# Performance work log

Measured on AMD Instinct MI355X. Metric: run time of the kernel, lower is better.

The kernel has to match this reference:

```python
import jax, jax.numpy as jnp
import numpy as np

BS, C, N, L = 2, 64, 400, 12   # [bs, c, N, L]
D, H = 128, 8                  # model_dim, num_heads
HD = D // H                    # head_dim = 16
FF = 1024                      # feed_forward_dim
EPS_LN = 1e-5
EPS_NORM = 1e-12


def setup_inputs() -> dict:
    key = jax.random.key(0)
    ks = jax.random.split(key, 24)
    w = lambda k, shape: jax.random.normal(k, shape, jnp.float32) * 0.02
    inp = {
        "x":     jax.random.normal(ks[0], (BS, C, N, L), jnp.float32),
        "x_au1": jax.random.normal(ks[1], (BS, C, N, L), jnp.float32),
        "x_au2": jax.random.normal(ks[2], (BS, C, N, L), jnp.float32),
        # projections stored as [in, out] so y = x @ W + b
        "WQ1": w(ks[3], (C, D)),  "bQ1": jnp.zeros((D,)),
        "WQ2": w(ks[4], (C, D)),  "bQ2": jnp.zeros((D,)),
        "WK1": w(ks[5], (C, D)),  "bK1": jnp.zeros((D,)),
        "WK2": w(ks[6], (C, D)),  "bK2": jnp.zeros((D,)),
        "WV":  w(ks[7], (C, D)),  "bV":  jnp.zeros((D,)),
        "Wo":  w(ks[8], (D, C)),  "bo":  jnp.zeros((C,)),
        "Wf1": w(ks[9], (C, FF)), "bf1": jnp.zeros((FF,)),
        "Wf2": w(ks[10], (FF, C)),"bf2": jnp.zeros((C,)),
        "g1": jnp.ones((C,)), "be1": jnp.zeros((C,)),
        "g2": jnp.ones((C,)), "be2": jnp.zeros((C,)),
        "temperature": jnp.ones((H,)),
        "alphas": jnp.ones((2,)) / 2.0,
    }
    return inp


def _layernorm(x, g, b):
    m = jnp.mean(x, axis=-1, keepdims=True)
    v = jnp.var(x, axis=-1, keepdims=True)
    return (x - m) * jax.lax.rsqrt(v + EPS_LN) * g + b


def _l2norm(x):
    n = jnp.linalg.norm(x, axis=-1, keepdims=True)
    return x / jnp.maximum(n, EPS_NORM)


def _topk_masked(attn, k):
    # keep entries >= k-th largest along last axis (ties measure-zero for floats)
    kth = jax.lax.top_k(attn, k)[0][..., -1:]
    return jnp.where(attn >= kth, attn, -jnp.inf)


def reference(x, x_au1, x_au2, WQ1, bQ1, WQ2, bQ2, WK1, bK1, WK2, bK2,
              WV, bV, Wo, bo, Wf1, bf1, Wf2, bf2, g1, be1, g2, be2,
              temperature, alphas):
    # [bs,c,N,L] -> [bs,L,N,c]
    xt  = jnp.transpose(x,     (0, 3, 2, 1))
    a1t = jnp.transpose(x_au1, (0, 3, 2, 1))
    a2t = jnp.transpose(x_au2, (0, 3, 2, 1))
    bs, Lq, Nq, c = xt.shape

    def heads(t):  # [bs,L,N,D] -> [bs,L,N,H,hd]
        return t.reshape(bs, Lq, Nq, H, HD)

    q1 = _l2norm(heads(a1t @ WQ1 + bQ1))
    q2 = _l2norm(heads(a2t @ WQ2 + bQ2))
    k1 = _l2norm(heads(xt  @ WK1 + bK1))
    k2 = _l2norm(heads(xt  @ WK2 + bK2))
    v  = heads(xt @ WV + bV)

    # dual cosine attention scores: [bs,H,L,N,N]
    attn = (jnp.einsum('blnhd,blmhd->bhlnm', q1, k1)
            + jnp.einsum('blnhd,blmhd->bhlnm', q2, k2))
    attn = attn * temperature.reshape(1, H, 1, 1, 1)

    k_top1 = max(1, Nq // 2)
    k_top2 = max(1, Nq // 4)
    p1 = jax.nn.softmax(_topk_masked(attn, k_top1), axis=-1)
    p2 = jax.nn.softmax(_topk_masked(attn, k_top2), axis=-1)

    out1 = jnp.einsum('bhlnm,blmhd->blnhd', p1, v)
    out2 = jnp.einsum('bhlnm,blmhd->blnhd', p2, v)
    al = jax.nn.softmax(alphas)
    out = (out1 * al[0] + out2 * al[1]).reshape(bs, Lq, Nq, D)

    out = out @ Wo + bo
    out = _layernorm(xt + out, g1, be1)
    ff = jax.nn.relu(out @ Wf1 + bf1) @ Wf2 + bf2
    out = _layernorm(out + ff, g2, be2)
    out = jnp.transpose(out, (0, 3, 2, 1))  # back to [bs,c,N,L]

    attn_flat = attn.reshape(bs * H, Lq, Nq, Nq)
    p2_flat = p2.reshape(bs * H, Lq, Nq, Nq)
    return out, attn_flat, p2_flat
```

## Files before the change

### kernel.cpp

```cpp
#include <hip/hip_runtime.h>
#include <math.h>

#define BSZ 2
#define CHN 64
#define NPT 400
#define LW  12
#define DM  128
#define NH  8
#define HDM 16
#define FFD 1024
#define NTOK (BSZ*LW*NPT)

#define TA 16
__global__ __launch_bounds__(128) void stage_a(
    const float* __restrict__ x, const float* __restrict__ xa1, const float* __restrict__ xa2,
    const float* __restrict__ WQ1, const float* __restrict__ bQ1,
    const float* __restrict__ WQ2, const float* __restrict__ bQ2,
    const float* __restrict__ WK1, const float* __restrict__ bK1,
    const float* __restrict__ WK2, const float* __restrict__ bK2,
    const float* __restrict__ WV,  const float* __restrict__ bV,
    float* __restrict__ q1n, float* __restrict__ q2n,
    float* __restrict__ k1n, float* __restrict__ k2n, float* __restrict__ vv)
{
  __shared__ float xv[TA][CHN], a1v[TA][CHN], a2v[TA][CHN];
  const int tid = threadIdx.x;
  const int t0 = blockIdx.x * TA;
  for (int i = tid; i < TA*CHN; i += 128) {
    int tt = i & (TA-1), c = i >> 4;
    int token = t0 + tt;
    int n = token % NPT; int bl = token / NPT; int l = bl % LW; int b = bl / LW;
    int gidx = ((b*CHN + c)*NPT + n)*LW + l;
    xv[tt][c] = x[gidx]; a1v[tt][c] = xa1[gidx]; a2v[tt][c] = xa2[gidx];
  }
  __syncthreads();
  const int d = tid;
  float aq1[TA], aq2[TA], ak1[TA], ak2[TA], av[TA];
  float b1 = bQ1[d], b2 = bQ2[d], b3 = bK1[d], b4 = bK2[d], b5 = bV[d];
  #pragma unroll
  for (int t = 0; t < TA; ++t) { aq1[t]=b1; aq2[t]=b2; ak1[t]=b3; ak2[t]=b4; av[t]=b5; }
  for (int c = 0; c < CHN; ++c) {
    float w1 = WQ1[c*DM + d], w2 = WQ2[c*DM + d], w3 = WK1[c*DM + d],
          w4 = WK2[c*DM + d], w5 = WV[c*DM + d];
    #pragma unroll
    for (int t = 0; t < TA; ++t) {
      float xc = xv[t][c], x1 = a1v[t][c], x2 = a2v[t][c];
      aq1[t] += x1*w1; aq2[t] += x2*w2; ak1[t] += xc*w3; ak2[t] += xc*w4; av[t] += xc*w5;
    }
  }
  const int h = d >> 4, dd = d & 15;
  #pragma unroll
  for (int t = 0; t < TA; ++t) {
    float s1 = aq1[t]*aq1[t], s2 = aq2[t]*aq2[t], s3 = ak1[t]*ak1[t], s4 = ak2[t]*ak2[t];
    #pragma unroll
    for (int m = 1; m < 16; m <<= 1) {
      s1 += __shfl_xor(s1, m); s2 += __shfl_xor(s2, m);
      s3 += __shfl_xor(s3, m); s4 += __shfl_xor(s4, m);
    }
    float i1 = 1.f/fmaxf(sqrtf(s1),1e-12f), i2 = 1.f/fmaxf(sqrtf(s2),1e-12f),
          i3 = 1.f/fmaxf(sqrtf(s3),1e-12f), i4 = 1.f/fmaxf(sqrtf(s4),1e-12f);
    int token = t0 + t;
    int n = token % NPT; int bl = token / NPT; int l = bl % LW; int b = bl / LW;
    int base = (((b*LW + l)*NH + h)*NPT + n)*HDM + dd;
    q1n[base] = aq1[t]*i1; q2n[base] = aq2[t]*i2;
    k1n[base] = ak1[t]*i3; k2n[base] = ak2[t]*i4; vv[base] = av[t];
  }
}

__device__ __forceinline__ unsigned okey(float xf) {
  unsigned u = __float_as_uint(xf);
  return (u & 0x80000000u) ? ~u : (u | 0x80000000u);
}

__global__ __launch_bounds__(256, 2) void stage_b(
    const float* __restrict__ q1n, const float* __restrict__ q2n,
    const float* __restrict__ k1n, const float* __restrict__ k2n,
    const float* __restrict__ vv,
    const float* __restrict__ temperature, const float* __restrict__ alphas,
    float* __restrict__ attn_o, float* __restrict__ p2_o, float* __restrict__ oa)
{
  __shared__ float4 k1s[4*401], k2s[4*401], vs[4*401];
  int wg = blockIdx.x;
  const int s = wg & 3; wg >>= 2;
  const int l = wg % LW; wg /= LW;
  const int h = wg & 7; const int b = wg >> 3;
  const int tid = threadIdx.x, lane = tid & 63, wave = tid >> 6;

  const int slice = (b*LW + l)*NH + h;
  const int oslice = (b*NH + h)*LW + l;
  const float4* k1g = (const float4*)(k1n + slice*NPT*HDM);
  const float4* k2g = (const float4*)(k2n + slice*NPT*HDM);
  const float4* vg  = (const float4*)(vv  + slice*NPT*HDM);
  for (int i = tid; i < NPT*4; i += 256) {
    int m = i >> 2, w4 = i & 3;
    k1s[w4*401 + m] = k1g[i];
    k2s[w4*401 + m] = k2g[i];
    vs [w4*401 + m] = vg[i];
  }
  __syncthreads();

  const float temp = temperature[h];
  float a0 = alphas[0], a1 = alphas[1];
  float amx = fmaxf(a0, a1);
  float e0 = __expf(a0 - amx), e1 = __expf(a1 - amx);
  float al0 = e0/(e0+e1), al1 = e1/(e0+e1);

  const float* q1base = q1n + slice*NPT*HDM;
  const float* q2base = q2n + slice*NPT*HDM;
  float* attn_base = attn_o + (size_t)oslice*NPT*NPT;
  float* p2_base   = p2_o   + (size_t)oslice*NPT*NPT;
  const int tokbase = (b*LW + l)*NPT;

  for (int bi = wave; bi < 25; bi += 4) {
    const int nb = s*100 + bi*4;
    float sc[4][7];
    #pragma unroll
    for (int r = 0; r < 4; ++r)
      #pragma unroll
      for (int j = 0; j < 7; ++j) sc[r][j] = 0.f;

    #pragma unroll
    for (int ch = 0; ch < 4; ++ch) {
      float4 q1c[4], q2c[4];
      #pragma unroll
      for (int r = 0; r < 4; ++r) {
        q1c[r] = *(const float4*)(q1base + (nb+r)*HDM + ch*4);
        q2c[r] = *(const float4*)(q2base + (nb+r)*HDM + ch*4);
      }
      #pragma unroll
      for (int j = 0; j < 7; ++j) {
        int m = lane + 64*j;
        if (j < 6 || lane < 16) {
          float4 kc1 = k1s[ch*401 + m];
          float4 kc2 = k2s[ch*401 + m];
          #pragma unroll
          for (int r = 0; r < 4; ++r) {
            sc[r][j] += q1c[r].x*kc1.x + q1c[r].y*kc1.y + q1c[r].z*kc1.z + q1c[r].w*kc1.w
                      + q2c[r].x*kc2.x + q2c[r].y*kc2.y + q2c[r].z*kc2.z + q2c[r].w*kc2.w;
          }
        }
      }
    }
    #pragma unroll
    for (int r = 0; r < 4; ++r) {
      #pragma unroll
      for (int j = 0; j < 7; ++j) {
        sc[r][j] *= temp;
        int m = lane + 64*j;
        if (j < 6 || lane < 16) attn_base[(nb + r)*NPT + m] = sc[r][j];
      }
    }
    #pragma unroll
    for (int r = 0; r < 4; ++r) {
      unsigned key[7];
      #pragma unroll
      for (int j = 0; j < 7; ++j) {
        bool valid = (j < 6) || (lane < 16);
        key[j] = valid ? okey(sc[r][j]) : 0u;
      }
      float am = -3.4e38f;
      #pragma unroll
      for (int j = 0; j < 7; ++j) if ((j < 6) || (lane < 16)) am = fmaxf(am, sc[r][j]);
      #pragma unroll
      for (int m2 = 1; m2 < 64; m2 <<= 1) am = fmaxf(am, __shfl_xor(am, m2));

      unsigned v1 = 0u, v2 = 0u;
      {
        unsigned prefix = 0u;
        #pragma clang loop unroll(disable)
        for (int bit = 31; bit >= 0; --bit) {
          unsigned T = prefix | (1u << bit);
          int cnt = 0;
          #pragma unroll
          for (int j = 0; j < 7; ++j) cnt += __popcll(__ballot(key[j] >= T));
          if (cnt >= 200) { prefix = T; if (cnt == 200) break; }
        }
        v1 = prefix;
      }
      {
        unsigned prefix = 0u;
        #pragma clang loop unroll(disable)
        for (int bit = 31; bit >= 0; --bit) {
          unsigned T = prefix | (1u << bit);
          int cnt = 0;
          #pragma unroll
          for (int j = 0; j < 7; ++j) cnt += __popcll(__ballot(key[j] >= T));
          if (cnt >= 100) { prefix = T; if (cnt == 100) break; }
        }
        v2 = prefix;
      }
      float e[7]; float s1 = 0.f, s2 = 0.f;
      #pragma unroll
      for (int j = 0; j < 7; ++j) {
        e[j] = ((j < 6) || (lane < 16)) ? __expf(sc[r][j] - am) : 0.f;
        s1 += (key[j] >= v1) ? e[j] : 0.f;
        s2 += (key[j] >= v2) ? e[j] : 0.f;
      }
      #pragma unroll
      for (int m2 = 1; m2 < 64; m2 <<= 1) { s1 += __shfl_xor(s1, m2); s2 += __shfl_xor(s2, m2); }
      float rz1 = 1.f / s1, rz2 = 1.f / s2;
      float c1 = al0 * rz1, c2 = al1 * rz2;
      #pragma unroll
      for (int j = 0; j < 7; ++j) {
        int m = lane + 64*j;
        float p2v = (key[j] >= v2) ? e[j]*rz2 : 0.f;
        if ((j < 6) || (lane < 16)) p2_base[(nb + r)*NPT + m] = p2v;
        sc[r][j] = e[j] * (((key[j] >= v1) ? c1 : 0.f) + ((key[j] >= v2) ? c2 : 0.f));
      }
    }
    float buf[64];
    #pragma unroll
    for (int i = 0; i < 64; ++i) buf[i] = 0.f;
    #pragma unroll
    for (int j = 0; j < 7; ++j) {
      int m = lane + 64*j;
      if (j < 6 || lane < 16) {
        float4 w0 = vs[0*401+m], w1 = vs[1*401+m], w2 = vs[2*401+m], w3 = vs[3*401+m];
        #pragma unroll
        for (int r = 0; r < 4; ++r) {
          float wr = sc[r][j];
          buf[r*16+ 0] += wr*w0.x; buf[r*16+ 1] += wr*w0.y; buf[r*16+ 2] += wr*w0.z; buf[r*16+ 3] += wr*w0.w;
          buf[r*16+ 4] += wr*w1.x; buf[r*16+ 5] += wr*w1.y; buf[r*16+ 6] += wr*w1.z; buf[r*16+ 7] += wr*w1.w;
          buf[r*16+ 8] += wr*w2.x; buf[r*16+ 9] += wr*w2.y; buf[r*16+10] += wr*w2.z; buf[r*16+11] += wr*w2.w;
          buf[r*16+12] += wr*w3.x; buf[r*16+13] += wr*w3.y; buf[r*16+14] += wr*w3.z; buf[r*16+15] += wr*w3.w;
        }
      }
    }
    #pragma unroll
    for (int st = 0; st < 6; ++st) {
      int bsel = (lane >> st) & 1;
      #pragma unroll
      for (int u = 0; u < (64 >> (st+1)); ++u) {
        float lo = buf[2*u], hi = buf[2*u+1];
        float keep = bsel ? hi : lo;
        float send = bsel ? lo : hi;
        float recv = __shfl_xor(send, 1 << st);
        buf[u] = keep + recv;
      }
    }
    int rr = lane >> 4, ddd = lane & 15;
    oa[(tokbase + nb + rr)*DM + h*HDM + ddd] = buf[0];
  }
}

#define TC 32
__global__ __launch_bounds__(256, 2) void stage_c(
    const float* __restrict__ oa, const float* __restrict__ x,
    const float* __restrict__ Wo, const float* __restrict__ bo,
    const float* __restrict__ Wf1, const float* __restrict__ bf1,
    const float* __restrict__ Wf2, const float* __restrict__ bf2,
    const float* __restrict__ g1, const float* __restrict__ be1,
    const float* __restrict__ g2, const float* __restrict__ be2,
    float* __restrict__ outp)
{
  __shared__ float4 oa_lds[TC*32];
  __shared__ float4 y1_lds[TC*16];
  __shared__ float4 act_lds[TC*64];
  const int tid = threadIdx.x;
  const int t0 = blockIdx.x * TC;
  const float4* oag = (const float4*)(oa + t0*DM);
  for (int i = tid; i < TC*32; i += 256) oa_lds[i] = oag[i];
  __syncthreads();

  const int c = tid & 63, g = tid >> 6;
  float bo_c = bo[c], g1c = g1[c], be1c = be1[c], g2c = g2[c], be2c = be2[c], bf2c = bf2[c];

  float o1[8];
  #pragma unroll
  for (int k = 0; k < 8; ++k) o1[k] = bo_c;
  for (int d4 = 0; d4 < 32; ++d4) {
    float w0 = Wo[(4*d4+0)*CHN + c];
    float w1 = Wo[(4*d4+1)*CHN + c];
    float w2 = Wo[(4*d4+2)*CHN + c];
    float w3 = Wo[(4*d4+3)*CHN + c];
    #pragma unroll
    for (int k = 0; k < 8; ++k) {
      float4 u = oa_lds[(g + 4*k)*32 + d4];
      o1[k] += u.x*w0 + u.y*w1 + u.z*w2 + u.w*w3;
    }
  }
  float y1r[8];
  #pragma unroll
  for (int k = 0; k < 8; ++k) {
    int token = t0 + g + 4*k;
    int n = token % NPT; int bl = token / NPT; int l = bl % LW; int b = bl / LW;
    float val = o1[k] + x[((b*CHN + c)*NPT + n)*LW + l];
    float sm = val, sq = val*val;
    #pragma unroll
    for (int m2 = 1; m2 < 64; m2 <<= 1) { sm += __shfl_xor(sm, m2); sq += __shfl_xor(sq, m2); }
    float mean = sm * (1.f/64.f);
    float var = sq * (1.f/64.f) - mean*mean;
    float y = (val - mean) * rsqrtf(var + 1e-5f) * g1c + be1c;
    y1r[k] = y;
    ((float*)y1_lds)[(g + 4*k)*CHN + c] = y;
  }
  __syncthreads();

  float o2a[8];
  #pragma unroll
  for (int k = 0; k < 8; ++k) o2a[k] = 0.f;

  for (int fb = 0; fb < 4; ++fb) {
    {
      const int ft = tid & 63, ga = tid >> 6;
      const int f = fb*256 + ft*4;
      float4 facc[8];
      float4 bb = *(const float4*)(bf1 + f);
      #pragma unroll
      for (int k = 0; k < 8; ++k) facc[k] = bb;
      for (int c4 = 0; c4 < 16; ++c4) {
        float4 w0 = *(const float4*)(Wf1 + (4*c4+0)*FFD + f);
        float4 w1 = *(const float4*)(Wf1 + (4*c4+1)*FFD + f);
        float4 w2 = *(const float4*)(Wf1 + (4*c4+2)*FFD + f);
        float4 w3 = *(const float4*)(Wf1 + (4*c4+3)*FFD + f);
        #pragma unroll
        for (int k = 0; k < 8; ++k) {
          float4 y4 = y1_lds[(ga + 4*k)*16 + c4];
          facc[k].x += y4.x*w0.x + y4.y*w1.x + y4.z*w2.x + y4.w*w3.x;
          facc[k].y += y4.x*w0.y + y4.y*w1.y + y4.z*w2.y + y4.w*w3.y;
          facc[k].z += y4.x*w0.z + y4.y*w1.z + y4.z*w2.z + y4.w*w3.z;
          facc[k].w += y4.x*w0.w + y4.y*w1.w + y4.z*w2.w + y4.w*w3.w;
        }
      }
      #pragma unroll
      for (int k = 0; k < 8; ++k) {
        float4 rv;
        rv.x = fmaxf(facc[k].x, 0.f); rv.y = fmaxf(facc[k].y, 0.f);
        rv.z = fmaxf(facc[k].z, 0.f); rv.w = fmaxf(facc[k].w, 0.f);
        act_lds[(ga + 4*k)*64 + ft] = rv;
      }
    }
    __syncthreads();
    for (int f4 = 0; f4 < 64; ++f4) {
      int f = fb*256 + f4*4;
      float w0 = Wf2[(f+0)*CHN + c];
      float w1 = Wf2[(f+1)*CHN + c];
      float w2 = Wf2[(f+2)*CHN + c];
      float w3 = Wf2[(f+3)*CHN + c];
      #pragma unroll
      for (int k = 0; k < 8; ++k) {
        float4 a4 = act_lds[(g + 4*k)*64 + f4];
        o2a[k] += a4.x*w0 + a4.y*w1 + a4.z*w2 + a4.w*w3;
      }
    }
    __syncthreads();
  }
  #pragma unroll
  for (int k = 0; k < 8; ++k) {
    int token = t0 + g + 4*k;
    int n = token % NPT; int bl = token / NPT; int l = bl % LW; int b = bl / LW;
    float val = y1r[k] + o2a[k] + bf2c;
    float sm = val, sq = val*val;
    #pragma unroll
    for (int m2 = 1; m2 < 64; m2 <<= 1) { sm += __shfl_xor(sm, m2); sq += __shfl_xor(sq, m2); }
    float mean = sm * (1.f/64.f);
    float var = sq * (1.f/64.f) - mean*mean;
    float y = (val - mean) * rsqrtf(var + 1e-5f) * g2c + be2c;
    outp[((b*CHN + c)*NPT + n)*LW + l] = y;
  }
}

extern "C" void kernel_launch(void* const* d_in, const int* in_sizes, int n_in,
                              void* d_out, int out_size, void* d_ws, size_t ws_size,
                              hipStream_t stream) {
  const float* x    = (const float*)d_in[0];
  const float* xa1  = (const float*)d_in[1];
  const float* xa2  = (const float*)d_in[2];
  const float* WQ1  = (const float*)d_in[3];
  const float* bQ1  = (const float*)d_in[4];
  const float* WQ2  = (const float*)d_in[5];
  const float* bQ2  = (const float*)d_in[6];
  const float* WK1  = (const float*)d_in[7];
  const float* bK1  = (const float*)d_in[8];
  const float* WK2  = (const float*)d_in[9];
  const float* bK2  = (const float*)d_in[10];
  const float* WV   = (const float*)d_in[11];
  const float* bV   = (const float*)d_in[12];
  const float* Wo   = (const float*)d_in[13];
  const float* bo   = (const float*)d_in[14];
  const float* Wf1  = (const float*)d_in[15];
  const float* bf1  = (const float*)d_in[16];
  const float* Wf2  = (const float*)d_in[17];
  const float* bf2  = (const float*)d_in[18];
  const float* g1   = (const float*)d_in[19];
  const float* be1  = (const float*)d_in[20];
  const float* g2   = (const float*)d_in[21];
  const float* be2  = (const float*)d_in[22];
  const float* temp = (const float*)d_in[23];
  const float* alph = (const float*)d_in[24];

  float* outp   = (float*)d_out;
  float* attn_o = outp + (size_t)BSZ*CHN*NPT*LW;
  float* p2_o   = attn_o + (size_t)BSZ*NH*LW*NPT*NPT;

  const size_t SLICE = (size_t)BSZ*LW*NH*NPT*HDM;
  float* w   = (float*)d_ws;
  float* q1n = w;             w += SLICE;
  float* q2n = w;             w += SLICE;
  float* k1n = w;             w += SLICE;
  float* k2n = w;             w += SLICE;
  float* vv  = w;             w += SLICE;
  float* oa  = w;             w += (size_t)NTOK*DM;

  stage_a<<<NTOK/TA, 128, 0, stream>>>(x, xa1, xa2, WQ1, bQ1, WQ2, bQ2,
                                       WK1, bK1, WK2, bK2, WV, bV,
                                       q1n, q2n, k1n, k2n, vv);
  stage_b<<<BSZ*NH*LW*4, 256, 0, stream>>>(q1n, q2n, k1n, k2n, vv,
                                           temp, alph, attn_o, p2_o, oa);
  stage_c<<<NTOK/TC, 256, 0, stream>>>(oa, x, Wo, bo, Wf1, bf1, Wf2, bf2,
                                       g1, be1, g2, be2, outp);
}
```

Before: 1.296 ms.

## Reorder token indexing to (n,l), vectorize IO, fuse dual top-k search, drop V LDS

Changes the token ordering in stage_a and stage_c from (b,l,n) to (b,n,l), so the inputs and output in [bs,c,N,L] layout are read and written as contiguous float4 rows staged through padded shared memory instead of strided scalar accesses. In stage_b, the two radix-select loops for the top-200 and top-100 thresholds are merged into one loop. That loop starts at the highest bit where the row max and min keys differ, and the max comes from the key reduction. V is no longer copied to LDS and is read straight from global memory, which frees LDS so occupancy can rise to 3 blocks per CU. The risks are more global traffic for V reads and correctness depending on the matching token-order change in oa.

```diff
diff --git a/kernel.cpp b/kernel.cpp
--- a/kernel.cpp
+++ b/kernel.cpp
@@ -22,15 +22,24 @@
     float* __restrict__ q1n, float* __restrict__ q2n,
     float* __restrict__ k1n, float* __restrict__ k2n, float* __restrict__ vv)
 {
-  __shared__ float xv[TA][CHN], a1v[TA][CHN], a2v[TA][CHN];
+  __shared__ float xv[TA][65], a1v[TA][65], a2v[TA][65];
   const int tid = threadIdx.x;
   const int t0 = blockIdx.x * TA;
-  for (int i = tid; i < TA*CHN; i += 128) {
-    int tt = i & (TA-1), c = i >> 4;
-    int token = t0 + tt;
-    int n = token % NPT; int bl = token / NPT; int l = bl % LW; int b = bl / LW;
-    int gidx = ((b*CHN + c)*NPT + n)*LW + l;
-    xv[tt][c] = x[gidx]; a1v[tt][c] = xa1[gidx]; a2v[tt][c] = xa2[gidx];
+  const int b  = t0 / 4800;
+  const int nl0 = t0 % 4800;
+  {
+    const float4* xg  = (const float4*)x;
+    const float4* a1g = (const float4*)xa1;
+    const float4* a2g = (const float4*)xa2;
+    for (int i = tid; i < 256; i += 128) {
+      int c = i >> 2, q = i & 3;
+      int src = ((b*64 + c)*4800 + nl0)/4 + q;
+      float4 xq = xg[src], a1q = a1g[src], a2q = a2g[src];
+      int tt = q*4;
+      xv[tt+0][c]=xq.x;  xv[tt+1][c]=xq.y;  xv[tt+2][c]=xq.z;  xv[tt+3][c]=xq.w;
+      a1v[tt+0][c]=a1q.x; a1v[tt+1][c]=a1q.y; a1v[tt+2][c]=a1q.z; a1v[tt+3][c]=a1q.w;
+      a2v[tt+0][c]=a2q.x; a2v[tt+1][c]=a2q.y; a2v[tt+2][c]=a2q.z; a2v[tt+3][c]=a2q.w;
+    }
   }
   __syncthreads();
   const int d = tid;
@@ -58,8 +67,8 @@
     }
     float i1 = 1.f/fmaxf(sqrtf(s1),1e-12f), i2 = 1.f/fmaxf(sqrtf(s2),1e-12f),
           i3 = 1.f/fmaxf(sqrtf(s3),1e-12f), i4 = 1.f/fmaxf(sqrtf(s4),1e-12f);
-    int token = t0 + t;
-    int n = token % NPT; int bl = token / NPT; int l = bl % LW; int b = bl / LW;
+    int nl = nl0 + t;
+    int n = nl / 12, l = nl % 12;
     int base = (((b*LW + l)*NH + h)*NPT + n)*HDM + dd;
     q1n[base] = aq1[t]*i1; q2n[base] = aq2[t]*i2;
     k1n[base] = ak1[t]*i3; k2n[base] = ak2[t]*i4; vv[base] = av[t];
@@ -70,15 +79,19 @@
   unsigned u = __float_as_uint(xf);
   return (u & 0x80000000u) ? ~u : (u | 0x80000000u);
 }
-
-__global__ __launch_bounds__(256, 2) void stage_b(
+__device__ __forceinline__ float dekey(unsigned k) {
+  unsigned u = (k & 0x80000000u) ? (k & 0x7FFFFFFFu) : ~k;
+  return __uint_as_float(u);
+}
+
+__global__ __launch_bounds__(256, 3) void stage_b(
     const float* __restrict__ q1n, const float* __restrict__ q2n,
     const float* __restrict__ k1n, const float* __restrict__ k2n,
     const float* __restrict__ vv,
     const float* __restrict__ temperature, const float* __restrict__ alphas,
     float* __restrict__ attn_o, float* __restrict__ p2_o, float* __restrict__ oa)
 {
-  __shared__ float4 k1s[4*401], k2s[4*401], vs[4*401];
+  __shared__ float4 k1s[4*401], k2s[4*401];
   int wg = blockIdx.x;
   const int s = wg & 3; wg >>= 2;
   const int l = wg % LW; wg /= LW;
@@ -94,7 +107,6 @@
     int m = i >> 2, w4 = i & 3;
     k1s[w4*401 + m] = k1g[i];
     k2s[w4*401 + m] = k2g[i];
-    vs [w4*401 + m] = vg[i];
   }
   __syncthreads();
 
@@ -108,7 +120,6 @@
   const float* q2base = q2n + slice*NPT*HDM;
   float* attn_base = attn_o + (size_t)oslice*NPT*NPT;
   float* p2_base   = p2_o   + (size_t)oslice*NPT*NPT;
-  const int tokbase = (b*LW + l)*NPT;
 
   for (int bi = wave; bi < 25; bi += 4) {
     const int nb = s*100 + bi*4;
@@ -152,59 +163,68 @@
     #pragma unroll
     for (int r = 0; r < 4; ++r) {
       unsigned key[7];
+      unsigned kmx = 0u, kmn = 0xFFFFFFFFu;
       #pragma unroll
       for (int j = 0; j < 7; ++j) {
         bool valid = (j < 6) || (lane < 16);
-        key[j] = valid ? okey(sc[r][j]) : 0u;
-      }
-      float am = -3.4e38f;
-      #pragma unroll
-      for (int j = 0; j < 7; ++j) if ((j < 6) || (lane < 16)) am = fmaxf(am, sc[r][j]);
-      #pragma unroll
-      for (int m2 = 1; m2 < 64; m2 <<= 1) am = fmaxf(am, __shfl_xor(am, m2));
-
-      unsigned v1 = 0u, v2 = 0u;
-      {
-        unsigned prefix = 0u;
+        unsigned kk = valid ? okey(sc[r][j]) : 0u;
+        key[j] = kk;
+        kmx = kk > kmx ? kk : kmx;
+        unsigned kn = valid ? kk : 0xFFFFFFFFu;
+        kmn = kn < kmn ? kn : kmn;
+      }
+      #pragma unroll
+      for (int m2 = 1; m2 < 64; m2 <<= 1) {
+        unsigned ox = __shfl_xor(kmx, m2); kmx = ox > kmx ? ox : kmx;
+        unsigned on = __shfl_xor(kmn, m2); kmn = on < kmn ? on : kmn;
+      }
+      float am = dekey(kmx);
+      unsigned diff = kmx ^ kmn;
+      unsigned p1, p2u;
+      if (diff == 0u) {
+        p1 = kmx; p2u = kmx;
+      } else {
+        int fd = 31 - __clz(diff);
+        unsigned hi = (fd >= 31) ? 0u : (~0u << (fd+1));
+        p1 = kmx & hi; p2u = p1;
+        bool d1 = false, d2 = false;
         #pragma clang loop unroll(disable)
-        for (int bit = 31; bit >= 0; --bit) {
-          unsigned T = prefix | (1u << bit);
-          int cnt = 0;
-          #pragma unroll
-          for (int j = 0; j < 7; ++j) cnt += __popcll(__ballot(key[j] >= T));
-          if (cnt >= 200) { prefix = T; if (cnt == 200) break; }
+        for (int bit = fd; bit >= 0; --bit) {
+          unsigned msk = 1u << bit;
+          if (!d1) {
+            unsigned T1 = p1 | msk;
+            int c1 = 0;
+            #pragma unroll
+            for (int j = 0; j < 7; ++j) c1 += __popcll(__ballot(key[j] >= T1));
+            if (c1 >= 200) { p1 = T1; d1 = (c1 == 200); }
+          }
+          if (!d2) {
+            unsigned T2 = p2u | msk;
+            int c2 = 0;
+            #pragma unroll
+            for (int j = 0; j < 7; ++j) c2 += __popcll(__ballot(key[j] >= T2));
+            if (c2 >= 100) { p2u = T2; d2 = (c2 == 100); }
+          }
+          if (d1 & d2) break;
         }
-        v1 = prefix;
-      }
-      {
-        unsigned prefix = 0u;
-        #pragma clang loop unroll(disable)
-        for (int bit = 31; bit >= 0; --bit) {
-          unsigned T = prefix | (1u << bit);
-          int cnt = 0;
-          #pragma unroll
-          for (int j = 0; j < 7; ++j) cnt += __popcll(__ballot(key[j] >= T));
-          if (cnt >= 100) { prefix = T; if (cnt == 100) break; }
-        }
-        v2 = prefix;
       }
       float e[7]; float s1 = 0.f, s2 = 0.f;
       #pragma unroll
       for (int j = 0; j < 7; ++j) {
         e[j] = ((j < 6) || (lane < 16)) ? __expf(sc[r][j] - am) : 0.f;
-        s1 += (key[j] >= v1) ? e[j] : 0.f;
-        s2 += (key[j] >= v2) ? e[j] : 0.f;
+        s1 += (key[j] >= p1)  ? e[j] : 0.f;
+        s2 += (key[j] >= p2u) ? e[j] : 0.f;
       }
       #pragma unroll
       for (int m2 = 1; m2 < 64; m2 <<= 1) { s1 += __shfl_xor(s1, m2); s2 += __shfl_xor(s2, m2); }
       float rz1 = 1.f / s1, rz2 = 1.f / s2;
-      float c1 = al0 * rz1, c2 = al1 * rz2;
+      float c1f = al0 * rz1, c2f = al1 * rz2;
       #pragma unroll
       for (int j = 0; j < 7; ++j) {
         int m = lane + 64*j;
-        float p2v = (key[j] >= v2) ? e[j]*rz2 : 0.f;
+        float p2v = (key[j] >= p2u) ? e[j]*rz2 : 0.f;
         if ((j < 6) || (lane < 16)) p2_base[(nb + r)*NPT + m] = p2v;
-        sc[r][j] = e[j] * (((key[j] >= v1) ? c1 : 0.f) + ((key[j] >= v2) ? c2 : 0.f));
+        sc[r][j] = e[j] * (((key[j] >= p1) ? c1f : 0.f) + ((key[j] >= p2u) ? c2f : 0.f));
       }
     }
     float buf[64];
@@ -214,7 +234,8 @@
     for (int j = 0; j < 7; ++j) {
       int m = lane + 64*j;
       if (j < 6 || lane < 16) {
-        float4 w0 = vs[0*401+m], w1 = vs[1*401+m], w2 = vs[2*401+m], w3 = vs[3*401+m];
+        const float4* vp = vg + m*4;
+        float4 w0 = vp[0], w1 = vp[1], w2 = vp[2], w3 = vp[3];
         #pragma unroll
         for (int r = 0; r < 4; ++r) {
           float wr = sc[r][j];
@@ -238,7 +259,7 @@
       }
     }
     int rr = lane >> 4, ddd = lane & 15;
-    oa[(tokbase + nb + rr)*DM + h*HDM + ddd] = buf[0];
+    oa[((size_t)b*4800 + (size_t)(nb + rr)*12 + l)*DM + h*HDM + ddd] = buf[0];
   }
 }
 
@@ -253,12 +274,23 @@
     float* __restrict__ outp)
 {
   __shared__ float4 oa_lds[TC*32];
+  __shared__ float  xs[TC][65];
   __shared__ float4 y1_lds[TC*16];
   __shared__ float4 act_lds[TC*64];
   const int tid = threadIdx.x;
   const int t0 = blockIdx.x * TC;
+  const int b = t0 / 4800, nl0 = t0 % 4800;
   const float4* oag = (const float4*)(oa + t0*DM);
   for (int i = tid; i < TC*32; i += 256) oa_lds[i] = oag[i];
+  {
+    const float4* xg = (const float4*)x;
+    for (int i = tid; i < 512; i += 256) {
+      int c = i >> 3, q = i & 7;
+      float4 xq = xg[((b*64 + c)*4800 + nl0)/4 + q];
+      int tt = q*4;
+      xs[tt+0][c]=xq.x; xs[tt+1][c]=xq.y; xs[tt+2][c]=xq.z; xs[tt+3][c]=xq.w;
+    }
+  }
   __syncthreads();
 
   const int c = tid & 63, g = tid >> 6;
@@ -281,9 +313,7 @@
   float y1r[8];
   #pragma unroll
   for (int k = 0; k < 8; ++k) {
-    int token = t0 + g + 4*k;
-    int n = token % NPT; int bl = token / NPT; int l = bl % LW; int b = bl / LW;
-    float val = o1[k] + x[((b*CHN + c)*NPT + n)*LW + l];
+    float val = o1[k] + xs[g + 4*k][c];
     float sm = val, sq = val*val;
     #pragma unroll
     for (int m2 = 1; m2 < 64; m2 <<= 1) { sm += __shfl_xor(sm, m2); sq += __shfl_xor(sq, m2); }
@@ -346,8 +376,6 @@
   }
   #pragma unroll
   for (int k = 0; k < 8; ++k) {
-    int token = t0 + g + 4*k;
-    int n = token % NPT; int bl = token / NPT; int l = bl % LW; int b = bl / LW;
     float val = y1r[k] + o2a[k] + bf2c;
     float sm = val, sq = val*val;
     #pragma unroll
@@ -355,7 +383,18 @@
     float mean = sm * (1.f/64.f);
     float var = sq * (1.f/64.f) - mean*mean;
     float y = (val - mean) * rsqrtf(var + 1e-5f) * g2c + be2c;
-    outp[((b*CHN + c)*NPT + n)*LW + l] = y;
+    xs[g + 4*k][c] = y;
+  }
+  __syncthreads();
+  {
+    float4* og = (float4*)outp;
+    for (int i = tid; i < 512; i += 256) {
+      int cc = i >> 3, q = i & 7;
+      int tt = q*4;
+      float4 yq;
+      yq.x = xs[tt+0][cc]; yq.y = xs[tt+1][cc]; yq.z = xs[tt+2][cc]; yq.w = xs[tt+3][cc];
+      og[((b*64 + cc)*4800 + nl0)/4 + q] = yq;
+    }
   }
 }
 
```

Measured after the change: 1.728 ms. +33.3%, slower.
